# Kernel tuning notes

Hardware: AMD Instinct MI355X
Metric: run time of the kernel (lower is better)

Reference implementation:

```python
import jax, jax.numpy as jnp
import numpy as np

N, E, H, NF, MN, ME = 4096, 65536, 128, 4, 8, 4
DEPTH, RATIO, NT = 5, 0.2, 2


def _k_list():
    ks, n = [], N
    for _ in range(DEPTH):
        n = int(np.ceil(RATIO * n))
        ks.append(n)
    return ks

K_LIST = _k_list()  # [820, 164, 33, 7, 2]


def _gcn(A, x, W, b, fill):
    # GCNConv on dense adjacency: D^-1/2 (A + fill*I) D^-1/2 @ (x W) + b
    n = A.shape[0]
    Ah = A + fill * jnp.eye(n, dtype=A.dtype)
    deg = jnp.sum(Ah, axis=1)
    dinv = jnp.where(deg > 0, jax.lax.rsqrt(jnp.maximum(deg, 1e-12)), 0.0)
    return (dinv[:, None] * Ah * dinv[None, :]) @ (x @ W) + b


def _augment(A):
    # GraphUNet.augment_adj: remove self loops, add weight-1 loops, A@A, remove self loops
    n = A.shape[0]
    eye = jnp.eye(n, dtype=A.dtype)
    A1 = A * (1.0 - eye) + eye
    A2 = A1 @ A1
    return A2 * (1.0 - eye)


def _topk_pool(A, x, w, k):
    # TopKPooling: score = tanh(x.w / ||w||), keep top-k, scale kept features by score
    score = jnp.tanh((x @ w) / jnp.linalg.norm(w))
    sv, perm = jax.lax.top_k(score, k)
    return x[perm] * sv[:, None], A[perm][:, perm], perm


def _graph_unet(A0, x, Wd0, bd0, Wd, bd, pool_w, Wu, bu):
    act = jax.nn.relu
    x = act(_gcn(A0, x, Wd0, bd0, 2.0))  # improved GCN: fill=2
    xs, As, perms = [x], [A0], []
    A = A0
    for i in range(DEPTH):
        A = _augment(A)
        x, A, perm = _topk_pool(A, x, pool_w[i], K_LIST[i])
        x = act(_gcn(A, x, Wd[i], bd[i], 2.0))
        if i < DEPTH - 1:
            xs.append(x)
            As.append(A)
        perms.append(perm)
    for i in range(DEPTH):
        j = DEPTH - 1 - i
        res, Aj, perm = xs[j], As[j], perms[j]
        up = jnp.zeros_like(res).at[perm].set(x)
        x = _gcn(Aj, res + up, Wu[i], bu[i], 2.0)  # sum_res=True
        if i < DEPTH - 1:
            x = act(x)
    return x


def _forward(F_0, mesh_node, mesh_edge, Wm, bm, Wd0, bd0, Wd, bd, pool_w,
             Wu, bu, Wout, bout, edge_index, n_time):
    src, dst = edge_index[0], edge_index[1]
    A = jnp.zeros((N, N), jnp.float32).at[dst, src].add(1.0)  # dst aggregates from src
    h = jnp.zeros((N, H), jnp.float32)
    F_cur = F_0
    Fs = []
    for _ in range(n_time):
        node_attr = jnp.concatenate([F_cur, mesh_node, h], axis=1)
        # Input: per-edge cat([x_i, x_j, e]) -> Linear -> scatter-sum by dst
        msg = jnp.concatenate([node_attr[dst], node_attr[src], mesh_edge], axis=1) @ Wm + bm
        h1 = jax.nn.relu(jax.ops.segment_sum(msg, dst, num_segments=N))
        h2 = _graph_unet(A, h1, Wd0, bd0, Wd, bd, pool_w, Wu, bu)
        h = jax.lax.stop_gradient(h2)
        h2 = jax.nn.relu(h2)
        F_next = _gcn(A, jnp.concatenate([h1, h2], axis=1), Wout, bout, 1.0)
        Fs.append(F_next)
        F_cur = jax.lax.stop_gradient(F_next)
    return jnp.stack(Fs, axis=1)  # [N, n_time, NF]


def setup_inputs() -> dict:
    key = jax.random.key(0)
    ks = jax.random.split(key, 12)
    s = 0.05
    node_in = NF + MN + H
    return {
        "F_0": jax.random.normal(ks[0], (N, NF), jnp.float32),
        "mesh_node": jax.random.normal(ks[1], (N, MN), jnp.float32),
        "mesh_edge": jax.random.normal(ks[2], (E, ME), jnp.float32),
        "Wm": jax.random.normal(ks[3], (2 * node_in + ME, H), jnp.float32) * s,
        "bm": jnp.zeros((H,), jnp.float32),
        "Wd0": jax.random.normal(ks[4], (H, H), jnp.float32) * s,
        "bd0": jnp.zeros((H,), jnp.float32),
        "Wd": jax.random.normal(ks[5], (DEPTH, H, H), jnp.float32) * s,
        "bd": jnp.zeros((DEPTH, H), jnp.float32),
        "pool_w": jax.random.normal(ks[6], (DEPTH, H), jnp.float32) * s,
        "Wu": jax.random.normal(ks[7], (DEPTH, H, H), jnp.float32) * s,
        "bu": jnp.zeros((DEPTH, H), jnp.float32),
        "Wout": jax.random.normal(ks[8], (2 * H, NF), jnp.float32) * s,
        "bout": jnp.zeros((NF,), jnp.float32),
        "edge_index": jax.random.randint(ks[9], (2, E), 0, N, dtype=jnp.int32),
        "n_time": NT,
    }


def reference(F_0, mesh_node, mesh_edge, Wm, bm, Wd0, bd0, Wd, bd, pool_w,
              Wu, bu, Wout, bout, edge_index, n_time):
    return _forward(F_0, mesh_node, mesh_edge, Wm, bm, Wd0, bd0, Wd, bd,
                    pool_w, Wu, bu, Wout, bout, edge_index, n_time)
```

## Files before the change

### kernel.cpp

```cpp
#include <hip/hip_runtime.h>
#include <math.h>

#define NN 4096
#define EE 65536
#define H 128
#define NF 4
#define MNODE 8
#define MEDGE 4
#define NT 2

__global__ void k_count(const int* __restrict__ dst, int* __restrict__ cnt) {
  int e = blockIdx.x * 256 + threadIdx.x;
  if (e < EE) atomicAdd(&cnt[dst[e]], 1);
}

__global__ void k_scan(const int* __restrict__ cnt, int* __restrict__ rp) {
  __shared__ int sh[1024];
  int t = threadIdx.x;
  int v0 = cnt[4*t], v1 = cnt[4*t+1], v2 = cnt[4*t+2], v3 = cnt[4*t+3];
  int p1 = v0, p2 = v0 + v1, p3 = p2 + v2, tot = p3 + v3;
  sh[t] = tot; __syncthreads();
  for (int off = 1; off < 1024; off <<= 1) {
    int add = (t >= off) ? sh[t-off] : 0;
    __syncthreads();
    sh[t] += add;
    __syncthreads();
  }
  int base = sh[t] - tot;
  rp[4*t] = base; rp[4*t+1] = base + p1; rp[4*t+2] = base + p2; rp[4*t+3] = base + p3;
  if (t == 1023) rp[NN] = sh[t];
}

__global__ void k_fill(const int* __restrict__ ei, int* __restrict__ cursor, int* __restrict__ cols) {
  int e = blockIdx.x * 256 + threadIdx.x;
  if (e < EE) {
    int d = ei[EE + e], s = ei[e];
    int pos = atomicAdd(&cursor[d], 1);
    cols[pos] = s;
  }
}

__global__ void k_dinv0(const int* __restrict__ cnt, float* __restrict__ d2, float* __restrict__ d1) {
  int i = blockIdx.x * 256 + threadIdx.x;
  if (i < NN) {
    float c = (float)cnt[i];
    d2[i] = 1.f / sqrtf(c + 2.f);
    d1[i] = 1.f / sqrtf(c + 1.f);
  }
}

__global__ void k_pwnorm(const float* __restrict__ pw, float* __restrict__ pwn) {
  int l = blockIdx.x, t = threadIdx.x;
  float a = pw[l*H + t], b = pw[l*H + 64 + t];
  float s = a*a + b*b;
  for (int off = 32; off > 0; off >>= 1) s += __shfl_down(s, off);
  if (t == 0) pwn[l] = sqrtf(s);
}

__global__ void k_segS(const int* __restrict__ dst, const float* __restrict__ me, float* __restrict__ S) {
  int e = blockIdx.x * 256 + threadIdx.x;
  if (e < EE) {
    int d = dst[e];
#pragma unroll
    for (int m = 0; m < MEDGE; m++) atomicAdd(&S[d*MEDGE + m], me[e*MEDGE + m]);
  }
}

__global__ void k_mm_cat(const float* __restrict__ F, const float* __restrict__ mn,
                         const float* __restrict__ h, const float* __restrict__ Wm,
                         float* __restrict__ P, float* __restrict__ Q) {
  __shared__ float as[140];
  int row = blockIdx.x, t = threadIdx.x;
  for (int c = t; c < 140; c += 128) {
    float v;
    if (c < NF) v = F[row*NF + c];
    else if (c < NF + MNODE) v = mn[row*MNODE + (c - NF)];
    else v = h[(size_t)row*H + (c - NF - MNODE)];
    as[c] = v;
  }
  __syncthreads();
  const float* BQ = Wm + 140*H;
  float ap = 0.f, aq = 0.f;
  for (int kk = 0; kk < 140; kk++) {
    float a = as[kk];
    ap += a * Wm[kk*H + t];
    aq += a * BQ[kk*H + t];
  }
  P[(size_t)row*H + t] = ap;
  Q[(size_t)row*H + t] = aq;
}

__global__ void k_spmm_h1_mm(const float* __restrict__ Q, const int* __restrict__ rp,
                             const int* __restrict__ cols, const float* __restrict__ Pm,
                             const float* __restrict__ bm, const float* __restrict__ S,
                             const float* __restrict__ WmB, const int* __restrict__ cnt,
                             const float* __restrict__ Wd0, const float* __restrict__ dinv2,
                             float* __restrict__ h1, float* __restrict__ tsb) {
  __shared__ float hs[128];
  int i = blockIdx.x, t = threadIdx.x;
  float acc = 0.f;
  int beg = rp[i], end = rp[i+1];
  for (int e = beg; e < end; e++) acc += Q[(size_t)cols[e]*H + t];
  float v = (float)cnt[i] * (Pm[(size_t)i*H + t] + bm[t]) + acc;
#pragma unroll
  for (int m = 0; m < MEDGE; m++) v += S[i*MEDGE + m] * WmB[m*H + t];
  v = fmaxf(v, 0.f);
  h1[(size_t)i*H + t] = v;
  hs[t] = v;
  __syncthreads();
  float a2 = 0.f;
  for (int kk = 0; kk < H; kk++) a2 += hs[kk] * Wd0[kk*H + t];
  tsb[(size_t)i*H + t] = a2 * dinv2[i];
}

__global__ void k_mm_rb(const float* __restrict__ A, int lda, const float* __restrict__ B,
                        float* __restrict__ C, int K, const float* __restrict__ dinv) {
  __shared__ float as[160];
  int row = blockIdx.x, t = threadIdx.x;
  float acc = 0.f;
  for (int k0 = 0; k0 < K; k0 += H) {
    int m = (K - k0 < H) ? (K - k0) : H;
    if (t < m) as[t] = A[(size_t)row*lda + k0 + t];
    __syncthreads();
    for (int kk = 0; kk < m; kk++) acc += as[kk] * B[(k0 + kk)*H + t];
    __syncthreads();
  }
  if (dinv) acc *= dinv[row];
  C[(size_t)row*H + t] = acc;
}

__global__ void k_spmm_fused(const float* __restrict__ ts, const int* __restrict__ rp,
                             const int* __restrict__ cols, const float* __restrict__ dinv,
                             float fill, const float* __restrict__ bias, int relu,
                             float* __restrict__ out) {
  int i = blockIdx.x, t = threadIdx.x;
  float acc = 0.f;
  int beg = rp[i], end = rp[i+1];
  for (int e = beg; e < end; e++) acc += ts[(size_t)cols[e]*H + t];
  float v;
  if (dinv) {
    v = dinv[i] * (acc + fill * ts[(size_t)i*H + t]) + bias[t];
    if (relu) v = fmaxf(v, 0.f);
  } else v = acc;
  out[(size_t)i*H + t] = v;
}

__global__ void k_score(const float* __restrict__ x, const float* __restrict__ pw,
                        const float* __restrict__ pwn, float* __restrict__ score,
                        unsigned long long* __restrict__ keys, int* __restrict__ rank) {
  int row = blockIdx.x, t = threadIdx.x;
  float s = x[(size_t)row*H + t]*pw[t] + x[(size_t)row*H + 64 + t]*pw[64 + t];
  for (int off = 32; off > 0; off >>= 1) s += __shfl_down(s, off);
  if (t == 0) {
    float sc = tanhf(s / pwn[0]);
    score[row] = sc;
    float s2 = sc + 0.0f;
    unsigned u = __float_as_uint(s2);
    u ^= (unsigned)(((int)u >> 31)) | 0x80000000u;
    keys[row] = ((unsigned long long)u << 12) | (unsigned)(4095 - row);
    rank[row] = 0;
  }
}

__global__ void k_count_rank(const unsigned long long* __restrict__ keys, int n,
                             int* __restrict__ rank) {
  __shared__ unsigned long long sk[256];
  int t = threadIdx.x;
  int j = blockIdx.y * 256 + t;
  sk[t] = (j < n) ? keys[j] : 0ull;
  __syncthreads();
  int i = blockIdx.x * 256 + t;
  if (i >= n) return;
  unsigned long long ki = keys[i];
  int r = 0;
#pragma unroll 8
  for (int jj = 0; jj < 256; jj++) r += (sk[jj] > ki) ? 1 : 0;
  if (r) atomicAdd(&rank[i], r);
}

__global__ void k_select(const float* __restrict__ score, const int* __restrict__ rank,
                         int n, int k, int* __restrict__ perm, float* __restrict__ sv,
                         int* __restrict__ inv) {
  int i = blockIdx.x * 256 + threadIdx.x;
  if (i < n) {
    int r = rank[i];
    inv[i] = r;
    if (r < k) { perm[r] = i; sv[r] = score[i]; }
  }
}

__global__ void k_poolx(const float* __restrict__ x, const int* __restrict__ perm,
                        const float* __restrict__ sv, float* __restrict__ xp) {
  int r = blockIdx.x, t = threadIdx.x;
  xp[(size_t)r*H + t] = x[(size_t)perm[r]*H + t] * sv[r];
}

__global__ void k_pool_small(const float* __restrict__ score, const unsigned long long* __restrict__ keys,
                             const float* __restrict__ x, int n, int k,
                             int* __restrict__ perm, float* __restrict__ sv,
                             int* __restrict__ inv, float* __restrict__ xp) {
  __shared__ unsigned long long ks[256];
  __shared__ int permS[40];
  __shared__ float svS[40];
  int t = threadIdx.x;
  ks[t] = (t < n) ? keys[t] : 0ull;
  __syncthreads();
  if (t < n) {
    unsigned long long ki = ks[t];
    int r = 0;
    for (int j = 0; j < n; j++) r += (ks[j] > ki) ? 1 : 0;
    inv[t] = r;
    if (r < k) {
      float sc = score[t];
      permS[r] = t; svS[r] = sc;
      perm[r] = t; sv[r] = sc;
    }
  }
  __syncthreads();
  for (int idx = t; idx < k*H; idx += 256) {
    int r = idx >> 7, c = idx & 127;
    xp[idx] = x[(size_t)permS[r]*H + c] * svS[r];
  }
}

__global__ void k_a820_f(const int* __restrict__ rp, const int* __restrict__ cols,
                         const int* __restrict__ perm, float* __restrict__ A820,
                         float* __restrict__ dv) {
  __shared__ float acc[NN];
  __shared__ float red[256];
  int r = blockIdx.x, t = threadIdx.x;
  for (int i = t; i < NN; i += 256) acc[i] = 0.f;
  __syncthreads();
  int pi = perm[r];
  int beg = rp[pi], end = rp[pi+1];
  for (int e = beg + t; e < end; e += 256) { int c = cols[e]; if (c != pi) atomicAdd(&acc[c], 1.f); }
  if (t == 0) atomicAdd(&acc[pi], 1.f);
  for (int e0 = beg; e0 < end; e0++) {
    int c = cols[e0];
    if (c == pi) continue;
    int b2 = rp[c], e2 = rp[c+1];
    for (int e = b2 + t; e < e2; e += 256) { int c2 = cols[e]; if (c2 != c) atomicAdd(&acc[c2], 1.f); }
    if (t == 0) atomicAdd(&acc[c], 1.f);
  }
  __syncthreads();
  float local = 0.f;
  for (int cc = t; cc < 820; cc += 256) {
    float val = (cc == r) ? 0.f : acc[perm[cc]];
    A820[(size_t)r*820 + cc] = val;
    local += val;
  }
  red[t] = local; __syncthreads();
  for (int off = 128; off > 0; off >>= 1) { if (t < off) red[t] += red[t+off]; __syncthreads(); }
  if (t == 0) dv[r] = 1.f / sqrtf(red[0] + 2.f);
}

__global__ void k_gathercols(const float* __restrict__ A, int n, const int* __restrict__ perm,
                             int knext, float* __restrict__ AP) {
  int idx = blockIdx.x * 256 + threadIdx.x;
  int total = n * knext;
  if (idx >= total) return;
  int kk = idx / knext, c = idx - kk * knext;
  AP[idx] = A[(size_t)kk * n + perm[c]];
}

__global__ void k_augpool2_f(const float* __restrict__ A, const float* __restrict__ AP,
                             int n, const int* __restrict__ perm, int knext,
                             float* __restrict__ out, float* __restrict__ dv) {
  __shared__ float rowb[832];
  __shared__ float red[256];
  int r = blockIdx.x, t = threadIdx.x;
  int pr = perm[r];
  for (int i = t; i < n; i += 256) rowb[i] = A[(size_t)pr*n + i];
  __syncthreads();
  float local = 0.f;
  for (int c = t; c < knext; c += 256) {
    float dot = 0.f;
#pragma unroll 8
    for (int kk = 0; kk < n; kk++) dot += rowb[kk] * AP[(size_t)kk*knext + c];
    float val = (c == r) ? 0.f : (dot + 2.f * AP[(size_t)pr*knext + c]);
    out[(size_t)r*knext + c] = val;
    local += val;
  }
  red[t] = local; __syncthreads();
  for (int off = 128; off > 0; off >>= 1) { if (t < off) red[t] += red[t+off]; __syncthreads(); }
  if (t == 0) dv[r] = 1.f / sqrtf(red[0] + 2.f);
}

__global__ void k_augpool_small(const float* __restrict__ A, int n, const int* __restrict__ perm,
                                int knext, float* __restrict__ out, float* __restrict__ dv) {
  __shared__ float rowb[256];
  __shared__ float rsum;
  int r = blockIdx.x, t = threadIdx.x;
  int pr = perm[r];
  if (t < n) rowb[t] = A[(size_t)pr*n + t];
  if (t == 0) rsum = 0.f;
  __syncthreads();
  int g = t >> 3, lane = t & 7;
  for (int c = g; c < knext; c += 32) {
    int pc = perm[c];
    float part = 0.f;
    for (int kk = lane; kk < n; kk += 8) part += rowb[kk] * A[(size_t)kk*n + pc];
    part += __shfl_down(part, 4, 8);
    part += __shfl_down(part, 2, 8);
    part += __shfl_down(part, 1, 8);
    if (lane == 0) {
      float val = (c == r) ? 0.f : (part + 2.f * rowb[pc]);
      out[(size_t)r*knext + c] = val;
      atomicAdd(&rsum, val);
    }
  }
  __syncthreads();
  if (t == 0) dv[r] = 1.f / sqrtf(rsum + 2.f);
}

__global__ void k_dense_gcn(const float* __restrict__ A, int n, const float* __restrict__ ts,
                            const float* __restrict__ dinv, float fill, const float* __restrict__ bias,
                            int relu, float* __restrict__ out) {
  int i = blockIdx.x, t = threadIdx.x;
  const float* Ar = A + (size_t)i * n;
  float acc = 0.f;
  int kk = 0;
  int n4 = n & ~3;
#pragma unroll 2
  for (; kk < n4; kk += 4) {
    float a0 = Ar[kk+0], a1 = Ar[kk+1], a2 = Ar[kk+2], a3 = Ar[kk+3];
    float t0 = ts[(size_t)(kk+0)*H + t];
    float t1 = ts[(size_t)(kk+1)*H + t];
    float t2 = ts[(size_t)(kk+2)*H + t];
    float t3 = ts[(size_t)(kk+3)*H + t];
    acc += a0*t0; acc += a1*t1; acc += a2*t2; acc += a3*t3;
  }
  for (; kk < n; kk++) acc += Ar[kk] * ts[(size_t)kk*H + t];
  float v = dinv[i] * (acc + fill * ts[(size_t)i*H + t]) + bias[t];
  if (relu) v = fmaxf(v, 0.f);
  out[(size_t)i*H + t] = v;
}

__global__ void k_upproj(const float* __restrict__ xs, const int* __restrict__ inv,
                         const float* __restrict__ xcur, int kk,
                         const float* __restrict__ W, const float* __restrict__ dinv,
                         float* __restrict__ tsb) {
  __shared__ float hs[128];
  int i = blockIdx.x, t = threadIdx.x;
  int r = inv[i];
  float v = xs[(size_t)i*H + t];
  if (r < kk) v += xcur[(size_t)r*H + t];
  hs[t] = v;
  __syncthreads();
  float acc = 0.f;
  for (int k2 = 0; k2 < H; k2++) acc += hs[k2] * W[k2*H + t];
  tsb[(size_t)i*H + t] = acc * dinv[i];
}

__global__ void k_outproj_r(const float* __restrict__ h1, const float* __restrict__ hbuf,
                            const float* __restrict__ Wout, const float* __restrict__ dinv1,
                            float* __restrict__ ts2) {
  int row = blockIdx.x, t = threadIdx.x;
  float p0 = 0.f, p1 = 0.f, p2 = 0.f, p3 = 0.f;
#pragma unroll
  for (int half = 0; half < 2; half++) {
    float a = h1[(size_t)row*H + half*64 + t];
    const float* w = Wout + (half*64 + t)*4;
    p0 += a*w[0]; p1 += a*w[1]; p2 += a*w[2]; p3 += a*w[3];
    float b = fmaxf(hbuf[(size_t)row*H + half*64 + t], 0.f);
    const float* w2 = Wout + (128 + half*64 + t)*4;
    p0 += b*w2[0]; p1 += b*w2[1]; p2 += b*w2[2]; p3 += b*w2[3];
  }
  for (int off = 32; off > 0; off >>= 1) {
    p0 += __shfl_down(p0, off); p1 += __shfl_down(p1, off);
    p2 += __shfl_down(p2, off); p3 += __shfl_down(p3, off);
  }
  if (t == 0) {
    float d = dinv1[row];
    ts2[row*4+0] = d*p0; ts2[row*4+1] = d*p1; ts2[row*4+2] = d*p2; ts2[row*4+3] = d*p3;
  }
}

__global__ void k_gcn_out(const float* __restrict__ ts2, const int* __restrict__ rp,
                          const int* __restrict__ cols, const float* __restrict__ dinv1,
                          const float* __restrict__ bout, float* __restrict__ Fcur,
                          float* __restrict__ dout, int tstep) {
  int i = blockIdx.x, t = threadIdx.x;
  int f = t & 3;
  float acc = 0.f;
  int beg = rp[i], end = rp[i+1];
  for (int e = beg + (t >> 2); e < end; e += 16) acc += ts2[cols[e]*4 + f];
  for (int off = 32; off >= 4; off >>= 1) acc += __shfl_down(acc, off);
  if (t < 4) {
    float v = dinv1[i] * (acc + ts2[i*4 + f]) + bout[f];
    Fcur[i*4 + f] = v;
    dout[i*(NT*NF) + tstep*NF + f] = v;
  }
}

extern "C" void kernel_launch(void* const* d_in, const int* in_sizes, int n_in,
                              void* d_out, int out_size, void* d_ws, size_t ws_size,
                              hipStream_t stream) {
  const float* F0        = (const float*)d_in[0];
  const float* mesh_node = (const float*)d_in[1];
  const float* mesh_edge = (const float*)d_in[2];
  const float* Wm        = (const float*)d_in[3];
  const float* bm        = (const float*)d_in[4];
  const float* Wd0       = (const float*)d_in[5];
  const float* bd0       = (const float*)d_in[6];
  const float* Wd        = (const float*)d_in[7];
  const float* bd        = (const float*)d_in[8];
  const float* pool_w    = (const float*)d_in[9];
  const float* Wu        = (const float*)d_in[10];
  const float* bu        = (const float*)d_in[11];
  const float* Wout      = (const float*)d_in[12];
  const float* bout      = (const float*)d_in[13];
  const int*   ei        = (const int*)d_in[14];
  float* out = (float*)d_out;

  char* p = (char*)d_ws;
  auto carve = [&](size_t bytes) -> char* {
    char* r = p;
    p += (bytes + 255) & ~(size_t)255;
    return r;
  };
  int*   cnt    = (int*)carve((size_t)NN*4);
  int*   rp     = (int*)carve((size_t)(NN+1)*4);
  int*   cursor = (int*)carve((size_t)NN*4);
  int*   cols   = (int*)carve((size_t)EE*4);
  int*   permb  = (int*)carve((size_t)5*832*4);
  float* svb    = (float*)carve((size_t)5*832*4);
  float* dinv2  = (float*)carve((size_t)NN*4);
  float* dinv1  = (float*)carve((size_t)NN*4);
  float* pwn    = (float*)carve(8*4);
  float* S      = (float*)carve((size_t)NN*MEDGE*4);
  int*   invb   = (int*)carve((size_t)5*NN*4);
  float* P      = (float*)carve((size_t)NN*H*4);
  float* Q      = (float*)carve((size_t)NN*H*4);
  float* h1     = (float*)carve((size_t)NN*H*4);
  float* hbuf   = (float*)carve((size_t)NN*H*4);
  float* tsb    = (float*)carve((size_t)NN*H*4);
  float* tmp    = (float*)carve((size_t)NN*H*4);
  float* x0     = (float*)carve((size_t)NN*H*4);
  float* x1     = (float*)carve((size_t)820*H*4);
  float* x2     = (float*)carve((size_t)164*H*4);
  float* x3     = (float*)carve((size_t)33*H*4);
  float* x4     = (float*)carve((size_t)7*H*4);
  float* xp     = (float*)carve((size_t)820*H*4);
  float* xcur   = (float*)carve((size_t)820*H*4);
  float* score  = (float*)carve((size_t)NN*4);
  unsigned long long* keysb = (unsigned long long*)carve((size_t)NN*8);
  int*   rankb  = (int*)carve((size_t)NN*4);
  float* A820   = (float*)carve((size_t)820*820*4);
  float* A164   = (float*)carve((size_t)164*164*4);
  float* A33    = (float*)carve((size_t)33*33*4);
  float* A7     = (float*)carve((size_t)7*7*4);
  float* A2b    = (float*)carve((size_t)2*2*4);
  float* dv820  = (float*)carve(820*4);
  float* dv164  = (float*)carve(164*4);
  float* dv33   = (float*)carve(33*4);
  float* dv7    = (float*)carve(7*4);
  float* dv2    = (float*)carve(2*4);
  float* ts2    = (float*)carve((size_t)NN*NF*4);
  float* Fcur   = (float*)carve((size_t)NN*NF*4);

  float* AP = tmp;

  const int KLh[5]  = {820, 164, 33, 7, 2};
  const int szs[5]  = {4096, 820, 164, 33, 7};
  float* Adense[5] = {A820, A164, A33, A7, A2b};
  float* dvl[5]    = {dv820, dv164, dv33, dv7, dv2};
  float* xsv[5]    = {x0, x1, x2, x3, x4};
  int* perml[5]; float* svl[5]; int* invl[5];
  for (int l = 0; l < 5; l++) {
    perml[l] = permb + l*832; svl[l] = svb + l*832; invl[l] = invb + l*NN;
  }

  hipMemsetAsync(cnt, 0, (size_t)NN*4, stream);
  hipMemsetAsync(S, 0, (size_t)NN*MEDGE*4, stream);
  hipMemsetAsync(hbuf, 0, (size_t)NN*H*4, stream);
  k_count<<<EE/256, 256, 0, stream>>>(ei + EE, cnt);
  k_scan<<<1, 1024, 0, stream>>>(cnt, rp);
  hipMemcpyAsync(cursor, rp, (size_t)NN*4, hipMemcpyDeviceToDevice, stream);
  k_fill<<<EE/256, 256, 0, stream>>>(ei, cursor, cols);
  k_dinv0<<<NN/256, 256, 0, stream>>>(cnt, dinv2, dinv1);
  k_pwnorm<<<5, 64, 0, stream>>>(pool_w, pwn);
  k_segS<<<EE/256, 256, 0, stream>>>(ei + EE, mesh_edge, S);
  hipMemcpyAsync(Fcur, F0, (size_t)NN*NF*4, hipMemcpyDeviceToDevice, stream);

  for (int step = 0; step < NT; step++) {
    k_mm_cat<<<NN, 128, 0, stream>>>(Fcur, mesh_node, hbuf, Wm, P, Q);
    k_spmm_h1_mm<<<NN, 128, 0, stream>>>(Q, rp, cols, P, bm, S, Wm + 280*H, cnt,
                                         Wd0, dinv2, h1, tsb);
    k_spmm_fused<<<NN, 128, 0, stream>>>(tsb, rp, cols, dinv2, 2.f, bd0, 1, x0);

    for (int i = 0; i < 5; i++) {
      int n_prev = szs[i], k = KLh[i];
      k_score<<<n_prev, 64, 0, stream>>>(xsv[i], pool_w + i*H, pwn + i, score, keysb, rankb);
      if (n_prev > 256) {
        int gb = (n_prev + 255) / 256;
        k_count_rank<<<dim3(gb, gb), 256, 0, stream>>>(keysb, n_prev, rankb);
        k_select<<<gb, 256, 0, stream>>>(score, rankb, n_prev, k, perml[i], svl[i], invl[i]);
        k_poolx<<<k, 128, 0, stream>>>(xsv[i], perml[i], svl[i], xp);
      } else {
        k_pool_small<<<1, 256, 0, stream>>>(score, keysb, xsv[i], n_prev, k,
                                            perml[i], svl[i], invl[i], xp);
      }
      if (i == 0) {
        k_a820_f<<<820, 256, 0, stream>>>(rp, cols, perml[0], A820, dv820);
      } else if (i == 1) {
        int tot = n_prev * k;
        k_gathercols<<<(tot + 255)/256, 256, 0, stream>>>(Adense[0], n_prev, perml[1], k, AP);
        k_augpool2_f<<<k, 256, 0, stream>>>(Adense[0], AP, n_prev, perml[1], k, Adense[1], dvl[1]);
      } else {
        k_augpool_small<<<k, 256, 0, stream>>>(Adense[i-1], n_prev, perml[i], k, Adense[i], dvl[i]);
      }
      k_mm_rb<<<k, 128, 0, stream>>>(xp, H, Wd + i*H*H, tsb, H, dvl[i]);
      float* outx = (i < 4) ? xsv[i+1] : xcur;
      k_dense_gcn<<<k, 128, 0, stream>>>(Adense[i], k, tsb, dvl[i], 2.f, bd + i*H, 1, outx);
    }

    for (int i = 0; i < 5; i++) {
      int j = 4 - i;
      int n = szs[j], kk = KLh[j];
      k_upproj<<<n, 128, 0, stream>>>(xsv[j], invl[j], xcur, kk, Wu + i*H*H,
                                      (j > 0) ? dvl[j-1] : dinv2, tsb);
      if (j > 0) {
        k_dense_gcn<<<n, 128, 0, stream>>>(Adense[j-1], n, tsb, dvl[j-1], 2.f, bu + i*H,
                                           (i < 4) ? 1 : 0, xcur);
      } else {
        k_spmm_fused<<<n, 128, 0, stream>>>(tsb, rp, cols, dinv2, 2.f, bu + i*H, 0, hbuf);
      }
    }

    k_outproj_r<<<NN, 64, 0, stream>>>(h1, hbuf, Wout, dinv1, ts2);
    k_gcn_out<<<NN, 64, 0, stream>>>(ts2, rp, cols, dinv1, bout, Fcur, out, step);
  }
}
```

Measured before the change: 800.5 us.

## Fuse score into GCN epilogues, pool-gather into matmul, deep levels into one block

Top-k pooling scores are now computed in the epilogue of the preceding GCN kernels, which removes the separate score launches. The pooled-feature gather is folded into the weight matmul. The three smallest U-Net levels (33, 7, 2 nodes), both down and up, run in a single 1024-thread kernel that keeps everything in shared memory, replacing many tiny launches. The trade-off is a serial single-block kernel with large per-thread register arrays (acc[33]), plus extra block syncs in the GCN kernels.

After: 890.1 us. +11.2%, slower.

```diff
diff --git a/kernel.cpp b/kernel.cpp
--- a/kernel.cpp
+++ b/kernel.cpp
@@ -63,6 +63,26 @@
     int d = dst[e];
 #pragma unroll
     for (int m = 0; m < MEDGE; m++) atomicAdd(&S[d*MEDGE + m], me[e*MEDGE + m]);
+  }
+}
+
+__device__ __forceinline__ void score_epilogue(float v, int row, int t,
+                                               const float* pw, const float* pwn1,
+                                               float* scoreo, unsigned long long* keyso,
+                                               int* ranko, float* r2) {
+  float sp = v * pw[t];
+  for (int off = 32; off > 0; off >>= 1) sp += __shfl_down(sp, off);
+  if ((t & 63) == 0) r2[t >> 6] = sp;
+  __syncthreads();
+  if (t == 0) {
+    float s = r2[0] + r2[1];
+    float sc = tanhf(s / pwn1[0]);
+    scoreo[row] = sc;
+    float s2 = sc + 0.0f;
+    unsigned u = __float_as_uint(s2);
+    u ^= (unsigned)(((int)u >> 31)) | 0x80000000u;
+    keyso[row] = ((unsigned long long)u << 12) | (unsigned)(4095 - row);
+    ranko[row] = 0;
   }
 }
 
@@ -113,26 +133,14 @@
   tsb[(size_t)i*H + t] = a2 * dinv2[i];
 }
 
-__global__ void k_mm_rb(const float* __restrict__ A, int lda, const float* __restrict__ B,
-                        float* __restrict__ C, int K, const float* __restrict__ dinv) {
-  __shared__ float as[160];
-  int row = blockIdx.x, t = threadIdx.x;
-  float acc = 0.f;
-  for (int k0 = 0; k0 < K; k0 += H) {
-    int m = (K - k0 < H) ? (K - k0) : H;
-    if (t < m) as[t] = A[(size_t)row*lda + k0 + t];
-    __syncthreads();
-    for (int kk = 0; kk < m; kk++) acc += as[kk] * B[(k0 + kk)*H + t];
-    __syncthreads();
-  }
-  if (dinv) acc *= dinv[row];
-  C[(size_t)row*H + t] = acc;
-}
-
 __global__ void k_spmm_fused(const float* __restrict__ ts, const int* __restrict__ rp,
                              const int* __restrict__ cols, const float* __restrict__ dinv,
                              float fill, const float* __restrict__ bias, int relu,
-                             float* __restrict__ out) {
+                             float* __restrict__ out,
+                             const float* __restrict__ pw, const float* __restrict__ pwn1,
+                             float* __restrict__ scoreo, unsigned long long* __restrict__ keyso,
+                             int* __restrict__ ranko) {
+  __shared__ float r2[2];
   int i = blockIdx.x, t = threadIdx.x;
   float acc = 0.f;
   int beg = rp[i], end = rp[i+1];
@@ -143,23 +151,7 @@
     if (relu) v = fmaxf(v, 0.f);
   } else v = acc;
   out[(size_t)i*H + t] = v;
-}
-
-__global__ void k_score(const float* __restrict__ x, const float* __restrict__ pw,
-                        const float* __restrict__ pwn, float* __restrict__ score,
-                        unsigned long long* __restrict__ keys, int* __restrict__ rank) {
-  int row = blockIdx.x, t = threadIdx.x;
-  float s = x[(size_t)row*H + t]*pw[t] + x[(size_t)row*H + 64 + t]*pw[64 + t];
-  for (int off = 32; off > 0; off >>= 1) s += __shfl_down(s, off);
-  if (t == 0) {
-    float sc = tanhf(s / pwn[0]);
-    score[row] = sc;
-    float s2 = sc + 0.0f;
-    unsigned u = __float_as_uint(s2);
-    u ^= (unsigned)(((int)u >> 31)) | 0x80000000u;
-    keys[row] = ((unsigned long long)u << 12) | (unsigned)(4095 - row);
-    rank[row] = 0;
-  }
+  if (pw) score_epilogue(v, i, t, pw, pwn1, scoreo, keyso, ranko, r2);
 }
 
 __global__ void k_count_rank(const unsigned long long* __restrict__ keys, int n,
@@ -189,38 +181,16 @@
   }
 }
 
-__global__ void k_poolx(const float* __restrict__ x, const int* __restrict__ perm,
-                        const float* __restrict__ sv, float* __restrict__ xp) {
-  int r = blockIdx.x, t = threadIdx.x;
-  xp[(size_t)r*H + t] = x[(size_t)perm[r]*H + t] * sv[r];
-}
-
-__global__ void k_pool_small(const float* __restrict__ score, const unsigned long long* __restrict__ keys,
-                             const float* __restrict__ x, int n, int k,
-                             int* __restrict__ perm, float* __restrict__ sv,
-                             int* __restrict__ inv, float* __restrict__ xp) {
-  __shared__ unsigned long long ks[256];
-  __shared__ int permS[40];
-  __shared__ float svS[40];
-  int t = threadIdx.x;
-  ks[t] = (t < n) ? keys[t] : 0ull;
-  __syncthreads();
-  if (t < n) {
-    unsigned long long ki = ks[t];
-    int r = 0;
-    for (int j = 0; j < n; j++) r += (ks[j] > ki) ? 1 : 0;
-    inv[t] = r;
-    if (r < k) {
-      float sc = score[t];
-      permS[r] = t; svS[r] = sc;
-      perm[r] = t; sv[r] = sc;
-    }
-  }
-  __syncthreads();
-  for (int idx = t; idx < k*H; idx += 256) {
-    int r = idx >> 7, c = idx & 127;
-    xp[idx] = x[(size_t)permS[r]*H + c] * svS[r];
-  }
+__global__ void k_mm_pool(const float* __restrict__ x, const int* __restrict__ perm,
+                          const float* __restrict__ sv, const float* __restrict__ B,
+                          float* __restrict__ C, const float* __restrict__ dinv) {
+  __shared__ float as[128];
+  int row = blockIdx.x, t = threadIdx.x;
+  as[t] = x[(size_t)perm[row]*H + t] * sv[row];
+  __syncthreads();
+  float acc = 0.f;
+  for (int kk = 0; kk < H; kk++) acc += as[kk] * B[kk*H + t];
+  C[(size_t)row*H + t] = acc * dinv[row];
 }
 
 __global__ void k_a820_f(const int* __restrict__ rp, const int* __restrict__ cols,
@@ -286,36 +256,13 @@
   if (t == 0) dv[r] = 1.f / sqrtf(red[0] + 2.f);
 }
 
-__global__ void k_augpool_small(const float* __restrict__ A, int n, const int* __restrict__ perm,
-                                int knext, float* __restrict__ out, float* __restrict__ dv) {
-  __shared__ float rowb[256];
-  __shared__ float rsum;
-  int r = blockIdx.x, t = threadIdx.x;
-  int pr = perm[r];
-  if (t < n) rowb[t] = A[(size_t)pr*n + t];
-  if (t == 0) rsum = 0.f;
-  __syncthreads();
-  int g = t >> 3, lane = t & 7;
-  for (int c = g; c < knext; c += 32) {
-    int pc = perm[c];
-    float part = 0.f;
-    for (int kk = lane; kk < n; kk += 8) part += rowb[kk] * A[(size_t)kk*n + pc];
-    part += __shfl_down(part, 4, 8);
-    part += __shfl_down(part, 2, 8);
-    part += __shfl_down(part, 1, 8);
-    if (lane == 0) {
-      float val = (c == r) ? 0.f : (part + 2.f * rowb[pc]);
-      out[(size_t)r*knext + c] = val;
-      atomicAdd(&rsum, val);
-    }
-  }
-  __syncthreads();
-  if (t == 0) dv[r] = 1.f / sqrtf(rsum + 2.f);
-}
-
 __global__ void k_dense_gcn(const float* __restrict__ A, int n, const float* __restrict__ ts,
                             const float* __restrict__ dinv, float fill, const float* __restrict__ bias,
-                            int relu, float* __restrict__ out) {
+                            int relu, float* __restrict__ out,
+                            const float* __restrict__ pw, const float* __restrict__ pwn1,
+                            float* __restrict__ scoreo, unsigned long long* __restrict__ keyso,
+                            int* __restrict__ ranko) {
+  __shared__ float r2[2];
   int i = blockIdx.x, t = threadIdx.x;
   const float* Ar = A + (size_t)i * n;
   float acc = 0.f;
@@ -334,6 +281,7 @@
   float v = dinv[i] * (acc + fill * ts[(size_t)i*H + t]) + bias[t];
   if (relu) v = fmaxf(v, 0.f);
   out[(size_t)i*H + t] = v;
+  if (pw) score_epilogue(v, i, t, pw, pwn1, scoreo, keyso, ranko, r2);
 }
 
 __global__ void k_upproj(const float* __restrict__ xs, const int* __restrict__ inv,
@@ -350,6 +298,315 @@
   float acc = 0.f;
   for (int k2 = 0; k2 < H; k2++) acc += hs[k2] * W[k2*H + t];
   tsb[(size_t)i*H + t] = acc * dinv[i];
+}
+
+__global__ __launch_bounds__(1024) void k_deep(
+    const float* __restrict__ x2, const float* __restrict__ A164,
+    const unsigned long long* __restrict__ keys2, const float* __restrict__ score2,
+    const float* __restrict__ pool_w, const float* __restrict__ pwn,
+    const float* __restrict__ Wd, const float* __restrict__ bd,
+    const float* __restrict__ Wu, const float* __restrict__ bu,
+    int* __restrict__ inv2_g, float* __restrict__ xcur_g) {
+  __shared__ float xp_s[33*128];
+  __shared__ float tsb_s[33*128];
+  __shared__ float x3s[33*128];
+  __shared__ float x4s[7*128];
+  __shared__ float xc_s[7*128];
+  __shared__ float A33s[33*33];
+  __shared__ float A7s[49];
+  __shared__ float A2s[4];
+  __shared__ float dv33s[33], dv7s[7], dv2s[2];
+  __shared__ int   perm33[33], perm7[7], perm2[2];
+  __shared__ int   inv33[33], inv7[7];
+  __shared__ float sv33[33], sv7[7], sv2[2];
+  __shared__ unsigned long long ksh[164];
+  __shared__ float scs[164];
+  const int NTH = 1024;
+  int t = threadIdx.x;
+
+  if (t < 164) { ksh[t] = keys2[t]; scs[t] = score2[t]; }
+  __syncthreads();
+  if (t < 164) {
+    unsigned long long ki = ksh[t];
+    int r = 0;
+    for (int j = 0; j < 164; j++) r += (ksh[j] > ki) ? 1 : 0;
+    inv2_g[t] = r;
+    if (r < 33) { perm33[r] = t; sv33[r] = scs[t]; }
+  }
+  __syncthreads();
+  for (int o = t; o < 33*128; o += NTH) {
+    int r = o >> 7, c = o & 127;
+    xp_s[o] = x2[(size_t)perm33[r]*H + c] * sv33[r];
+  }
+  for (int o = t; o < 33*33; o += NTH) {
+    int r = o / 33, c = o - r*33;
+    int pr = perm33[r], pc = perm33[c];
+    const float* Arw = A164 + (size_t)pr*164;
+    float dot = 0.f;
+    for (int kk = 0; kk < 164; kk++) dot += Arw[kk] * A164[(size_t)kk*164 + pc];
+    A33s[o] = (r == c) ? 0.f : (dot + 2.f * Arw[pc]);
+  }
+  __syncthreads();
+  if (t < 33) {
+    float s = 0.f;
+    for (int c = 0; c < 33; c++) s += A33s[t*33 + c];
+    dv33s[t] = 1.f / sqrtf(s + 2.f);
+  }
+  __syncthreads();
+  {
+    const float* Wd2 = Wd + 2*H*H;
+    if (t < 128) {
+      float acc[33];
+#pragma unroll
+      for (int r = 0; r < 33; r++) acc[r] = 0.f;
+      for (int kk = 0; kk < H; kk++) {
+        float w = Wd2[kk*H + t];
+#pragma unroll
+        for (int r = 0; r < 33; r++) acc[r] += xp_s[r*128 + kk] * w;
+      }
+#pragma unroll
+      for (int r = 0; r < 33; r++) tsb_s[r*128 + t] = acc[r] * dv33s[r];
+    }
+  }
+  __syncthreads();
+  {
+    const float* bd2 = bd + 2*H;
+    if (t < 128) {
+      float acc[33];
+#pragma unroll
+      for (int r = 0; r < 33; r++) acc[r] = 0.f;
+      for (int kk = 0; kk < 33; kk++) {
+        float tv = tsb_s[kk*128 + t];
+#pragma unroll
+        for (int r = 0; r < 33; r++) acc[r] += A33s[r*33 + kk] * tv;
+      }
+#pragma unroll
+      for (int r = 0; r < 33; r++) {
+        float v = dv33s[r] * (acc[r] + 2.f * tsb_s[r*128 + t]) + bd2[t];
+        x3s[r*128 + t] = fmaxf(v, 0.f);
+      }
+    }
+  }
+  __syncthreads();
+  if (t < 33) {
+    const float* pw3 = pool_w + 3*H;
+    float s = 0.f;
+    for (int c = 0; c < H; c++) s += x3s[t*128 + c] * pw3[c];
+    float sc = tanhf(s / pwn[3]);
+    scs[t] = sc;
+    float s2 = sc + 0.0f;
+    unsigned u = __float_as_uint(s2);
+    u ^= (unsigned)(((int)u >> 31)) | 0x80000000u;
+    ksh[t] = ((unsigned long long)u << 12) | (unsigned)(4095 - t);
+  }
+  __syncthreads();
+
+  if (t < 33) {
+    unsigned long long ki = ksh[t];
+    int r = 0;
+    for (int j = 0; j < 33; j++) r += (ksh[j] > ki) ? 1 : 0;
+    inv33[t] = r;
+    if (r < 7) { perm7[r] = t; sv7[r] = scs[t]; }
+  }
+  __syncthreads();
+  for (int o = t; o < 7*128; o += NTH) {
+    int r = o >> 7, c = o & 127;
+    xp_s[o] = x3s[perm7[r]*128 + c] * sv7[r];
+  }
+  for (int o = t; o < 49; o += NTH) {
+    int r = o / 7, c = o - r*7;
+    int pr = perm7[r], pc = perm7[c];
+    float dot = 0.f;
+    for (int kk = 0; kk < 33; kk++) dot += A33s[pr*33 + kk] * A33s[kk*33 + pc];
+    A7s[o] = (r == c) ? 0.f : (dot + 2.f * A33s[pr*33 + pc]);
+  }
+  __syncthreads();
+  if (t < 7) {
+    float s = 0.f;
+    for (int c = 0; c < 7; c++) s += A7s[t*7 + c];
+    dv7s[t] = 1.f / sqrtf(s + 2.f);
+  }
+  __syncthreads();
+  {
+    const float* Wd3 = Wd + 3*H*H;
+    if (t < 128) {
+      float acc[7];
+#pragma unroll
+      for (int r = 0; r < 7; r++) acc[r] = 0.f;
+      for (int kk = 0; kk < H; kk++) {
+        float w = Wd3[kk*H + t];
+#pragma unroll
+        for (int r = 0; r < 7; r++) acc[r] += xp_s[r*128 + kk] * w;
+      }
+#pragma unroll
+      for (int r = 0; r < 7; r++) tsb_s[r*128 + t] = acc[r] * dv7s[r];
+    }
+  }
+  __syncthreads();
+  {
+    const float* bd3 = bd + 3*H;
+    if (t < 128) {
+      float acc[7];
+#pragma unroll
+      for (int r = 0; r < 7; r++) acc[r] = 0.f;
+      for (int kk = 0; kk < 7; kk++) {
+        float tv = tsb_s[kk*128 + t];
+#pragma unroll
+        for (int r = 0; r < 7; r++) acc[r] += A7s[r*7 + kk] * tv;
+      }
+#pragma unroll
+      for (int r = 0; r < 7; r++) {
+        float v = dv7s[r] * (acc[r] + 2.f * tsb_s[r*128 + t]) + bd3[t];
+        x4s[r*128 + t] = fmaxf(v, 0.f);
+      }
+    }
+  }
+  __syncthreads();
+  if (t < 7) {
+    const float* pw4 = pool_w + 4*H;
+    float s = 0.f;
+    for (int c = 0; c < H; c++) s += x4s[t*128 + c] * pw4[c];
+    float sc = tanhf(s / pwn[4]);
+    scs[t] = sc;
+    float s2 = sc + 0.0f;
+    unsigned u = __float_as_uint(s2);
+    u ^= (unsigned)(((int)u >> 31)) | 0x80000000u;
+    ksh[t] = ((unsigned long long)u << 12) | (unsigned)(4095 - t);
+  }
+  __syncthreads();
+
+  if (t < 7) {
+    unsigned long long ki = ksh[t];
+    int r = 0;
+    for (int j = 0; j < 7; j++) r += (ksh[j] > ki) ? 1 : 0;
+    inv7[t] = r;
+    if (r < 2) { perm2[r] = t; sv2[r] = scs[t]; }
+  }
+  __syncthreads();
+  for (int o = t; o < 2*128; o += NTH) {
+    int r = o >> 7, c = o & 127;
+    xp_s[o] = x4s[perm2[r]*128 + c] * sv2[r];
+  }
+  for (int o = t; o < 4; o += NTH) {
+    int r = o >> 1, c = o & 1;
+    int pr = perm2[r], pc = perm2[c];
+    float dot = 0.f;
+    for (int kk = 0; kk < 7; kk++) dot += A7s[pr*7 + kk] * A7s[kk*7 + pc];
+    A2s[o] = (r == c) ? 0.f : (dot + 2.f * A7s[pr*7 + pc]);
+  }
+  __syncthreads();
+  if (t < 2) dv2s[t] = 1.f / sqrtf(A2s[t*2] + A2s[t*2+1] + 2.f);
+  __syncthreads();
+  {
+    const float* Wd4 = Wd + 4*H*H;
+    if (t < 128) {
+      float a0 = 0.f, a1 = 0.f;
+      for (int kk = 0; kk < H; kk++) {
+        float w = Wd4[kk*H + t];
+        a0 += xp_s[kk] * w;
+        a1 += xp_s[128 + kk] * w;
+      }
+      tsb_s[t] = a0 * dv2s[0];
+      tsb_s[128 + t] = a1 * dv2s[1];
+    }
+  }
+  __syncthreads();
+  {
+    const float* bd4 = bd + 4*H;
+    if (t < 128) {
+      float t0 = tsb_s[t], t1 = tsb_s[128 + t];
+      float v0 = dv2s[0] * ((A2s[0]*t0 + A2s[1]*t1) + 2.f*t0) + bd4[t];
+      float v1 = dv2s[1] * ((A2s[2]*t0 + A2s[3]*t1) + 2.f*t1) + bd4[t];
+      xc_s[t] = fmaxf(v0, 0.f);
+      xc_s[128 + t] = fmaxf(v1, 0.f);
+    }
+  }
+  __syncthreads();
+
+  for (int o = t; o < 7*128; o += NTH) {
+    int r = o >> 7, c = o & 127;
+    int rr = inv7[r];
+    float v = x4s[o];
+    if (rr < 2) v += xc_s[rr*128 + c];
+    xp_s[o] = v;
+  }
+  __syncthreads();
+  {
+    if (t < 128) {
+      float acc[7];
+#pragma unroll
+      for (int r = 0; r < 7; r++) acc[r] = 0.f;
+      for (int kk = 0; kk < H; kk++) {
+        float w = Wu[kk*H + t];
+#pragma unroll
+        for (int r = 0; r < 7; r++) acc[r] += xp_s[r*128 + kk] * w;
+      }
+#pragma unroll
+      for (int r = 0; r < 7; r++) tsb_s[r*128 + t] = acc[r] * dv7s[r];
+    }
+  }
+  __syncthreads();
+  {
+    if (t < 128) {
+      float acc[7];
+#pragma unroll
+      for (int r = 0; r < 7; r++) acc[r] = 0.f;
+      for (int kk = 0; kk < 7; kk++) {
+        float tv = tsb_s[kk*128 + t];
+#pragma unroll
+        for (int r = 0; r < 7; r++) acc[r] += A7s[r*7 + kk] * tv;
+      }
+#pragma unroll
+      for (int r = 0; r < 7; r++) {
+        float v = dv7s[r] * (acc[r] + 2.f * tsb_s[r*128 + t]) + bu[t];
+        xc_s[r*128 + t] = fmaxf(v, 0.f);
+      }
+    }
+  }
+  __syncthreads();
+
+  for (int o = t; o < 33*128; o += NTH) {
+    int r = o >> 7, c = o & 127;
+    int rr = inv33[r];
+    float v = x3s[o];
+    if (rr < 7) v += xc_s[rr*128 + c];
+    xp_s[o] = v;
+  }
+  __syncthreads();
+  {
+    const float* Wu1 = Wu + 1*H*H;
+    if (t < 128) {
+      float acc[33];
+#pragma unroll
+      for (int r = 0; r < 33; r++) acc[r] = 0.f;
+      for (int kk = 0; kk < H; kk++) {
+        float w = Wu1[kk*H + t];
+#pragma unroll
+        for (int r = 0; r < 33; r++) acc[r] += xp_s[r*128 + kk] * w;
+      }
+#pragma unroll
+      for (int r = 0; r < 33; r++) tsb_s[r*128 + t] = acc[r] * dv33s[r];
+    }
+  }
+  __syncthreads();
+  {
+    const float* bu1 = bu + 1*H;
+    if (t < 128) {
+      float acc[33];
+#pragma unroll
+      for (int r = 0; r < 33; r++) acc[r] = 0.f;
+      for (int kk = 0; kk < 33; kk++) {
+        float tv = tsb_s[kk*128 + t];
+#pragma unroll
+        for (int r = 0; r < 33; r++) acc[r] += A33s[r*33 + kk] * tv;
+      }
+#pragma unroll
+      for (int r = 0; r < 33; r++) {
+        float v = dv33s[r] * (acc[r] + 2.f * tsb_s[r*128 + t]) + bu1[t];
+        xcur_g[(size_t)r*H + t] = fmaxf(v, 0.f);
+      }
+    }
+  }
 }
 
 __global__ void k_outproj_r(const float* __restrict__ h1, const float* __restrict__ hbuf,
@@ -439,33 +696,19 @@
   float* x0     = (float*)carve((size_t)NN*H*4);
   float* x1     = (float*)carve((size_t)820*H*4);
   float* x2     = (float*)carve((size_t)164*H*4);
-  float* x3     = (float*)carve((size_t)33*H*4);
-  float* x4     = (float*)carve((size_t)7*H*4);
-  float* xp     = (float*)carve((size_t)820*H*4);
   float* xcur   = (float*)carve((size_t)820*H*4);
   float* score  = (float*)carve((size_t)NN*4);
   unsigned long long* keysb = (unsigned long long*)carve((size_t)NN*8);
   int*   rankb  = (int*)carve((size_t)NN*4);
   float* A820   = (float*)carve((size_t)820*820*4);
   float* A164   = (float*)carve((size_t)164*164*4);
-  float* A33    = (float*)carve((size_t)33*33*4);
-  float* A7     = (float*)carve((size_t)7*7*4);
-  float* A2b    = (float*)carve((size_t)2*2*4);
   float* dv820  = (float*)carve(820*4);
   float* dv164  = (float*)carve(164*4);
-  float* dv33   = (float*)carve(33*4);
-  float* dv7    = (float*)carve(7*4);
-  float* dv2    = (float*)carve(2*4);
   float* ts2    = (float*)carve((size_t)NN*NF*4);
   float* Fcur   = (float*)carve((size_t)NN*NF*4);
 
   float* AP = tmp;
 
-  const int KLh[5]  = {820, 164, 33, 7, 2};
-  const int szs[5]  = {4096, 820, 164, 33, 7};
-  float* Adense[5] = {A820, A164, A33, A7, A2b};
-  float* dvl[5]    = {dv820, dv164, dv33, dv7, dv2};
-  float* xsv[5]    = {x0, x1, x2, x3, x4};
   int* perml[5]; float* svl[5]; int* invl[5];
   for (int l = 0; l < 5; l++) {
     perml[l] = permb + l*832; svl[l] = svb + l*832; invl[l] = invb + l*NN;
@@ -487,46 +730,36 @@
     k_mm_cat<<<NN, 128, 0, stream>>>(Fcur, mesh_node, hbuf, Wm, P, Q);
     k_spmm_h1_mm<<<NN, 128, 0, stream>>>(Q, rp, cols, P, bm, S, Wm + 280*H, cnt,
                                          Wd0, dinv2, h1, tsb);
-    k_spmm_fused<<<NN, 128, 0, stream>>>(tsb, rp, cols, dinv2, 2.f, bd0, 1, x0);
-
-    for (int i = 0; i < 5; i++) {
-      int n_prev = szs[i], k = KLh[i];
-      k_score<<<n_prev, 64, 0, stream>>>(xsv[i], pool_w + i*H, pwn + i, score, keysb, rankb);
-      if (n_prev > 256) {
-        int gb = (n_prev + 255) / 256;
-        k_count_rank<<<dim3(gb, gb), 256, 0, stream>>>(keysb, n_prev, rankb);
-        k_select<<<gb, 256, 0, stream>>>(score, rankb, n_prev, k, perml[i], svl[i], invl[i]);
-        k_poolx<<<k, 128, 0, stream>>>(xsv[i], perml[i], svl[i], xp);
-      } else {
-        k_pool_small<<<1, 256, 0, stream>>>(score, keysb, xsv[i], n_prev, k,
-                                            perml[i], svl[i], invl[i], xp);
-      }
-      if (i == 0) {
-        k_a820_f<<<820, 256, 0, stream>>>(rp, cols, perml[0], A820, dv820);
-      } else if (i == 1) {
-        int tot = n_prev * k;
-        k_gathercols<<<(tot + 255)/256, 256, 0, stream>>>(Adense[0], n_prev, perml[1], k, AP);
-        k_augpool2_f<<<k, 256, 0, stream>>>(Adense[0], AP, n_prev, perml[1], k, Adense[1], dvl[1]);
-      } else {
-        k_augpool_small<<<k, 256, 0, stream>>>(Adense[i-1], n_prev, perml[i], k, Adense[i], dvl[i]);
-      }
-      k_mm_rb<<<k, 128, 0, stream>>>(xp, H, Wd + i*H*H, tsb, H, dvl[i]);
-      float* outx = (i < 4) ? xsv[i+1] : xcur;
-      k_dense_gcn<<<k, 128, 0, stream>>>(Adense[i], k, tsb, dvl[i], 2.f, bd + i*H, 1, outx);
-    }
-
-    for (int i = 0; i < 5; i++) {
-      int j = 4 - i;
-      int n = szs[j], kk = KLh[j];
-      k_upproj<<<n, 128, 0, stream>>>(xsv[j], invl[j], xcur, kk, Wu + i*H*H,
-                                      (j > 0) ? dvl[j-1] : dinv2, tsb);
-      if (j > 0) {
-        k_dense_gcn<<<n, 128, 0, stream>>>(Adense[j-1], n, tsb, dvl[j-1], 2.f, bu + i*H,
-                                           (i < 4) ? 1 : 0, xcur);
-      } else {
-        k_spmm_fused<<<n, 128, 0, stream>>>(tsb, rp, cols, dinv2, 2.f, bu + i*H, 0, hbuf);
-      }
-    }
+    k_spmm_fused<<<NN, 128, 0, stream>>>(tsb, rp, cols, dinv2, 2.f, bd0, 1, x0,
+                                         pool_w, pwn, score, keysb, rankb);
+
+    k_count_rank<<<dim3(16, 16), 256, 0, stream>>>(keysb, NN, rankb);
+    k_select<<<16, 256, 0, stream>>>(score, rankb, NN, 820, perml[0], svl[0], invl[0]);
+    k_a820_f<<<820, 256, 0, stream>>>(rp, cols, perml[0], A820, dv820);
+    k_mm_pool<<<820, 128, 0, stream>>>(x0, perml[0], svl[0], Wd, tsb, dv820);
+    k_dense_gcn<<<820, 128, 0, stream>>>(A820, 820, tsb, dv820, 2.f, bd, 1, x1,
+                                         pool_w + H, pwn + 1, score, keysb, rankb);
+
+    k_count_rank<<<dim3(4, 4), 256, 0, stream>>>(keysb, 820, rankb);
+    k_select<<<4, 256, 0, stream>>>(score, rankb, 820, 164, perml[1], svl[1], invl[1]);
+    k_gathercols<<<(820*164 + 255)/256, 256, 0, stream>>>(A820, 820, perml[1], 164, AP);
+    k_augpool2_f<<<164, 256, 0, stream>>>(A820, AP, 820, perml[1], 164, A164, dv164);
+    k_mm_pool<<<164, 128, 0, stream>>>(x1, perml[1], svl[1], Wd + 1*H*H, tsb, dv164);
+    k_dense_gcn<<<164, 128, 0, stream>>>(A164, 164, tsb, dv164, 2.f, bd + 1*H, 1, x2,
+                                         pool_w + 2*H, pwn + 2, score, keysb, rankb);
+
+    k_deep<<<1, 1024, 0, stream>>>(x2, A164, keysb, score, pool_w, pwn,
+                                   Wd, bd, Wu, bu, invl[2], xcur);
+
+    k_upproj<<<164, 128, 0, stream>>>(x2, invl[2], xcur, 33, Wu + 2*H*H, dv164, tsb);
+    k_dense_gcn<<<164, 128, 0, stream>>>(A164, 164, tsb, dv164, 2.f, bu + 2*H, 1, xcur,
+                                         nullptr, nullptr, nullptr, nullptr, nullptr);
+    k_upproj<<<820, 128, 0, stream>>>(x1, invl[1], xcur, 164, Wu + 3*H*H, dv820, tsb);
+    k_dense_gcn<<<820, 128, 0, stream>>>(A820, 820, tsb, dv820, 2.f, bu + 3*H, 1, xcur,
+                                         nullptr, nullptr, nullptr, nullptr, nullptr);
+    k_upproj<<<NN, 128, 0, stream>>>(x0, invl[0], xcur, 820, Wu + 4*H*H, dinv2, tsb);
+    k_spmm_fused<<<NN, 128, 0, stream>>>(tsb, rp, cols, dinv2, 2.f, bu + 4*H, 0, hbuf,
+                                         nullptr, nullptr, nullptr, nullptr, nullptr);
 
     k_outproj_r<<<NN, 64, 0, stream>>>(h1, hbuf, Wout, dinv1, ts2);
     k_gcn_out<<<NN, 64, 0, stream>>>(ts2, rp, cols, dinv1, bout, Fcur, out, step);
```
